# Optimization experiments

Hardware: AMD Instinct MI355X
Metric: run time of the kernel (lower is better)

Reference implementation:

```python
import jax, jax.numpy as jnp
import numpy as np

B, T, C, V, L, H, HS = 64, 256, 256, 65, 6, 8, 32


def _ln(x, g, b, eps=1e-5):
    mu = jnp.mean(x, axis=-1, keepdims=True)
    var = jnp.mean(jnp.square(x - mu), axis=-1, keepdims=True)
    return (x - mu) * jax.lax.rsqrt(var + eps) * g + b


def setup_inputs() -> dict:
    key = jax.random.key(0)
    ks = jax.random.split(key, 28)
    n = lambda k, s: jax.random.normal(k, s, dtype=jnp.float32) * 0.02
    return {
        "idx": jax.random.randint(ks[0], (B, T), 0, V),
        "targets": jax.random.randint(ks[1], (B, T), 0, V),
        "tok_emb": n(ks[2], (V, C)),
        "pos_emb": n(ks[3], (T, C)),
        "wq": n(ks[4], (L, H, C, HS)), "bq": n(ks[5], (L, H, HS)),
        "wk": n(ks[6], (L, H, C, HS)), "bk": n(ks[7], (L, H, HS)),
        "wv": n(ks[8], (L, H, C, HS)), "bv": n(ks[9], (L, H, HS)),
        "wo": n(ks[10], (L, C, C)), "bo": n(ks[11], (L, C)),
        "ln1_g": jnp.ones((L, C), jnp.float32), "ln1_b": jnp.zeros((L, C), jnp.float32),
        "w1": n(ks[12], (L, C, 4 * C)), "b1": n(ks[13], (L, 4 * C)),
        "w2": n(ks[14], (L, 4 * C, C)), "b2": n(ks[15], (L, C)),
        "ln2_g": jnp.ones((L, C), jnp.float32), "ln2_b": jnp.zeros((L, C), jnp.float32),
        "lnf_g": jnp.ones((C,), jnp.float32), "lnf_b": jnp.zeros((C,), jnp.float32),
        "lm_w": n(ks[16], (C, V)), "lm_b": n(ks[17], (V,)),
    }


def reference(idx, targets, tok_emb, pos_emb, wq, bq, wk, bk, wv, bv, wo, bo,
              ln1_g, ln1_b, w1, b1, w2, b2, ln2_g, ln2_b, lnf_g, lnf_b, lm_w, lm_b):
    Bc, Tc = idx.shape
    x = tok_emb[idx] + pos_emb[:Tc]  # [B,T,C]
    causal = jnp.tril(jnp.ones((Tc, Tc), dtype=bool))
    scale = C ** (-0.5)  # NOTE: original scales by n_embd**-0.5, not head_size
    for l in range(L):
        xn = _ln(x, ln1_g[l], ln1_b[l])
        q = jnp.einsum('btc,hcd->bhtd', xn, wq[l]) + bq[l][None, :, None, :]
        k = jnp.einsum('btc,hcd->bhtd', xn, wk[l]) + bk[l][None, :, None, :]
        v = jnp.einsum('btc,hcd->bhtd', xn, wv[l]) + bv[l][None, :, None, :]
        s = jnp.einsum('bhtd,bhsd->bhts', q, k) * scale
        s = jnp.where(causal, s, -jnp.inf)
        a = jax.nn.softmax(s, axis=-1)  # dropout is identity in eval
        o = jnp.einsum('bhts,bhsd->bhtd', a, v)
        o = o.transpose(0, 2, 1, 3).reshape(Bc, Tc, C)  # concat heads
        x = x + o @ wo[l] + bo[l]
        xn2 = _ln(x, ln2_g[l], ln2_b[l])
        h = jax.nn.relu(xn2 @ w1[l] + b1[l])
        x = x + h @ w2[l] + b2[l]
    x = _ln(x, lnf_g, lnf_b)
    logits = (x @ lm_w + lm_b).reshape(Bc * Tc, V)
    logp = jax.nn.log_softmax(logits, axis=-1)
    tgt = targets.reshape(-1)
    loss = -jnp.mean(logp[jnp.arange(Bc * Tc), tgt])
    return logits, loss
```

## Files before the change

### kernel.cpp

```cpp
#include <hip/hip_runtime.h>
#include <hip/hip_bf16.h>
#include <math.h>

#define BB 64
#define TT 256
#define CC 256
#define VV 65
#define LL 6
#define HH 8
#define BT (BB*TT)

typedef unsigned short u16;
typedef __attribute__((ext_vector_type(8))) _Float16 h8v;
typedef __attribute__((ext_vector_type(4))) float f4v;
typedef __attribute__((ext_vector_type(4))) unsigned short u16x4;

typedef const unsigned int __attribute__((address_space(1))) gu32;
typedef unsigned int       __attribute__((address_space(3))) lu32;

__device__ inline u16 f2h(float f) { _Float16 h = (_Float16)f; return *(u16*)&h; }

__device__ inline void gld_lds16(const void* g, void* l) {
    __builtin_amdgcn_global_load_lds((gu32*)g, (lu32*)l, 16, 0, 0);
}


__device__ inline void pack_dev(const float* __restrict__ src, u16* __restrict__ dst,
                                int K, int N, int NT, int KT, int id) {
    int perLayer = NT * KT * 8192;
    int l = id / perLayer; int rem = id - l * perLayer;
    int tile = rem >> 13, within = rem & 8191;
    int nT = tile / KT, kT = tile - nT * KT;
    int colIn = within >> 6, u = within & 63;
    int s = (u >> 3) ^ (colIn & 7);
    int k = kT * 64 + s * 8 + (u & 7);
    int n = nT * 128 + colIn;
    float v = (n < N) ? src[((size_t)l * K + k) * N + n] : 0.f;
    dst[((size_t)l * NT * KT + tile) * 8192 + within] = f2h(v);
}

#define E_QKV (LL*24*8192)
#define E_WO  (LL*8*8192)
#define E_W1  (LL*32*8192)
#define E_W2  (LL*32*8192)
#define E_LM  (4*8192)
#define E_QB  (LL*768)
#define E_TOT (E_QKV+E_WO+E_W1+E_W2+E_LM+E_QB)

__global__ __launch_bounds__(256)
void pack_all(const float* __restrict__ wq, const float* __restrict__ wk,
              const float* __restrict__ wv, const float* __restrict__ wo,
              const float* __restrict__ w1, const float* __restrict__ w2,
              const float* __restrict__ lmw,
              const float* __restrict__ bq, const float* __restrict__ bk,
              const float* __restrict__ bv,
              u16* __restrict__ qkvT, u16* __restrict__ woT, u16* __restrict__ w1T,
              u16* __restrict__ w2T, u16* __restrict__ lmT, float* __restrict__ Bp) {
    int id = blockIdx.x * 256 + threadIdx.x;
    if (id < E_QKV) {
        const int perLayer = 24 * 8192;
        int l = id / perLayer; int rem = id - l * perLayer;
        int tile = rem >> 13, within = rem & 8191;
        int nT = tile >> 2, kT = tile & 3;
        int colIn = within >> 6, u = within & 63;
        int s = (u >> 3) ^ (colIn & 7);
        int k = kT * 64 + s * 8 + (u & 7);
        int n = nT * 128 + colIn;
        int which = n >> 8, hd = n & 255, h = hd >> 5, d = hd & 31;
        const float* src = (which == 0) ? wq : (which == 1) ? wk : wv;
        float v = src[(((size_t)l * HH + h) * CC + k) * 32 + d];
        qkvT[((size_t)l * 24 + tile) * 8192 + within] = f2h(v);
        return;
    }
    id -= E_QKV;
    if (id < E_WO) { pack_dev(wo, woT, 256, 256, 2, 4, id); return; }
    id -= E_WO;
    if (id < E_W1) { pack_dev(w1, w1T, 256, 1024, 8, 4, id); return; }
    id -= E_W1;
    if (id < E_W2) { pack_dev(w2, w2T, 1024, 256, 2, 16, id); return; }
    id -= E_W2;
    if (id < E_LM) { pack_dev(lmw, lmT, 256, VV, 1, 4, id); return; }
    id -= E_LM;
    if (id < E_QB) {
        int l = id / 768, j = id % 768;
        int which = j >> 8, hd = j & 255, h = hd >> 5, d = hd & 31;
        const float* src = (which == 0) ? bq : (which == 1) ? bk : bv;
        Bp[id] = src[((size_t)l * HH + h) * 32 + d];
    }
}

__global__ __launch_bounds__(256)
void embed_kernel(const int* __restrict__ idx, const float* __restrict__ te,
                  const float* __restrict__ pe, float* __restrict__ x) {
    int i = blockIdx.x * blockDim.x + threadIdx.x;
    if (i >= BT * 64) return;
    int bt = i >> 6, c4 = i & 63;
    int tok = idx[bt];
    int t = bt & (TT - 1);
    float4 a = ((const float4*)te)[(size_t)tok * 64 + c4];
    float4 p = ((const float4*)pe)[(size_t)t * 64 + c4];
    float4 o; o.x = a.x + p.x; o.y = a.y + p.y; o.z = a.z + p.z; o.w = a.w + p.w;
    ((float4*)x)[i] = o;
}

__global__ __launch_bounds__(256)
void ln_kernel(const float* __restrict__ x, const float* __restrict__ g,
               const float* __restrict__ b, u16* __restrict__ outT) {
    int lane = threadIdx.x & 63;
    int wave = threadIdx.x >> 6;
    int row = blockIdx.x * 4 + wave;
    float4 v = ((const float4*)(x + (size_t)row * CC))[lane];
    float s = v.x + v.y + v.z + v.w;
    #pragma unroll
    for (int m = 1; m < 64; m <<= 1) s += __shfl_xor(s, m, 64);
    float mu = s * (1.f / CC);
    float dx = v.x - mu, dy = v.y - mu, dz = v.z - mu, dw = v.w - mu;
    float vs = dx * dx + dy * dy + dz * dz + dw * dw;
    #pragma unroll
    for (int m = 1; m < 64; m <<= 1) vs += __shfl_xor(vs, m, 64);
    float rs = rsqrtf(vs * (1.f / CC) + 1e-5f);
    float4 gv = ((const float4*)g)[lane];
    float4 bv = ((const float4*)b)[lane];
    float o[4];
    o[0] = dx * rs * gv.x + bv.x;
    o[1] = dy * rs * gv.y + bv.y;
    o[2] = dz * rs * gv.z + bv.z;
    o[3] = dw * rs * gv.w + bv.w;
    int rIn = row & 127, mT = row >> 7;
    int kT = lane >> 4;
    int kIn = (lane * 4) & 63;
    int slot = kIn >> 3, j = kIn & 7;
    size_t base = ((size_t)mT * 4 + kT) * 8192;
    int ub = rIn * 64 + ((slot ^ (rIn & 7)) << 3) + j;
    u16x4 hv;
    #pragma unroll
    for (int q = 0; q < 4; ++q) hv[q] = f2h(o[q]);
    *(u16x4*)(outT + base + ub) = hv;
}

template<int EPI>
__global__ __launch_bounds__(512, 4)
void gemm_mfma(const u16* __restrict__ At, const u16* __restrict__ Bt,
               const float* __restrict__ bias, float* __restrict__ Co,
               u16* __restrict__ CoT, int KTfull, int KTc, int NT, int N, int KTout) {
    __shared__ __align__(16) char lds[65536];
    int tid = threadIdx.x;
    int l = tid & 63, w = tid >> 6;
    int nwg = gridDim.x;
    int id = blockIdx.x;
    int cpx = nwg >> 3;
    id = (id & 7) * cpx + (id >> 3);
    int mT = id / NT, nT = id - mT * NT;
    int ktBase = blockIdx.y * KTc;

    const char* Abase = (const char*)(At + ((size_t)mT * KTfull + ktBase) * 8192);
    const char* Bbase = (const char*)(Bt + ((size_t)nT * KTfull + ktBase) * 8192);
    int wm = w >> 1, wn = w & 1;

    f4v acc[2][4];
    #pragma unroll
    for (int i = 0; i < 2; ++i)
        #pragma unroll
        for (int j = 0; j < 4; ++j) acc[i][j] = (f4v)0.f;

    int lrow = l & 15, lg = l >> 4;

    #define STAGE(buf, kt) {                                           \
        char* la = lds + (buf) * 32768 + w * 2048;                     \
        char* lb = lds + (buf) * 32768 + 16384 + w * 2048;             \
        const char* ga = Abase + (kt) * 16384 + w * 2048 + l * 16;     \
        const char* gb = Bbase + (kt) * 16384 + w * 2048 + l * 16;     \
        _Pragma("unroll")                                              \
        for (int j = 0; j < 2; ++j) {                                  \
            gld_lds16(ga + j * 1024, la + j * 1024);                   \
            gld_lds16(gb + j * 1024, lb + j * 1024);                   \
        } }

    STAGE(0, 0);
    __syncthreads();
    int cur = 0;
    for (int kt = 0; kt < KTc; ++kt) {
        if (kt + 1 < KTc) STAGE(cur ^ 1, kt + 1);
        const char* lb0 = lds + cur * 32768;
        #pragma unroll
        for (int kh = 0; kh < 2; ++kh) {
            h8v ah[2], bh[4];
            #pragma unroll
            for (int mi = 0; mi < 2; ++mi) {
                int rc = wm * 32 + mi * 16 + lrow;
                ah[mi] = *(const h8v*)(lb0 + rc * 128 + 16 * ((kh * 4 + lg) ^ (rc & 7)));
            }
            #pragma unroll
            for (int ni = 0; ni < 4; ++ni) {
                int rc = wn * 64 + ni * 16 + lrow;
                bh[ni] = *(const h8v*)(lb0 + 16384 + rc * 128 + 16 * ((kh * 4 + lg) ^ (rc & 7)));
            }
            #pragma unroll
            for (int mi = 0; mi < 2; ++mi)
                #pragma unroll
                for (int ni = 0; ni < 4; ++ni)
                    acc[mi][ni] = __builtin_amdgcn_mfma_f32_16x16x32_f16(ah[mi], bh[ni], acc[mi][ni], 0, 0, 0);
        }
        __syncthreads();
        cur ^= 1;
    }
    #undef STAGE

    int colbase = nT * 128 + wn * 64;
    if (EPI == 0) {
        #pragma unroll
        for (int mi = 0; mi < 2; ++mi) {
            int r0 = mT * 128 + wm * 32 + mi * 16 + lg * 4;
            #pragma unroll
            for (int ni = 0; ni < 4; ++ni) {
                int cg = colbase + ni * 16 + lrow;
                float bv = bias[cg];
                #pragma unroll
                for (int q = 0; q < 4; ++q)
                    CoT[(size_t)(r0 + q) * N + cg] = f2h(acc[mi][ni][q] + bv);
            }
        }
    } else if (EPI == 2) {
        #pragma unroll
        for (int mi = 0; mi < 2; ++mi) {
            int r0 = mT * 128 + wm * 32 + mi * 16 + lg * 4;
            #pragma unroll
            for (int ni = 0; ni < 4; ++ni) {
                int cg = colbase + ni * 16 + lrow;
                float bv = bias[cg];
                int kTo = cg >> 6, kIn = cg & 63;
                size_t tbase = ((size_t)mT * KTout + kTo) * 8192;
                #pragma unroll
                for (int q = 0; q < 4; ++q) {
                    int rIn = (r0 + q) & 127;
                    float f = fmaxf(acc[mi][ni][q] + bv, 0.f);
                    int ub = rIn * 64 + (((kIn >> 3) ^ (rIn & 7)) << 3) + (kIn & 7);
                    CoT[tbase + ub] = f2h(f);
                }
            }
        }
    } else if (EPI == 3) {
        #pragma unroll
        for (int mi = 0; mi < 2; ++mi) {
            int r0 = mT * 128 + wm * 32 + mi * 16 + lg * 4;
            #pragma unroll
            for (int ni = 0; ni < 4; ++ni) {
                int cg = colbase + ni * 16 + lrow;
                if (cg < VV) {
                    float bv = bias[cg];
                    #pragma unroll
                    for (int q = 0; q < 4; ++q)
                        Co[(size_t)(r0 + q) * VV + cg] = acc[mi][ni][q] + bv;
                }
            }
        }
    } else {
        #pragma unroll
        for (int mi = 0; mi < 2; ++mi) {
            int r0 = mT * 128 + wm * 32 + mi * 16 + lg * 4;
            #pragma unroll
            for (int ni = 0; ni < 4; ++ni) {
                int cg = colbase + ni * 16 + lrow;
                float bv = (ktBase == 0) ? bias[cg] : 0.f;
                #pragma unroll
                for (int q = 0; q < 4; ++q)
                    atomicAdd(Co + (size_t)(r0 + q) * N + cg, acc[mi][ni][q] + bv);
            }
        }
    }
}

__global__ __launch_bounds__(256)
void attn_mfma(const u16* __restrict__ qkv, u16* __restrict__ outT) {
    __shared__ __align__(16) char lds[42496];
    int bh = blockIdx.x;
    bh = (bh & 7) * 64 + (bh >> 3);
    int b = bh >> 3, h = bh & 7;
    const u16* base = qkv + (size_t)b * TT * 768;
    int tid = threadIdx.x;
    int w = tid >> 6, l = tid & 63;
    int li = l & 15, g = l >> 4;

    {
        int r0 = tid >> 3, c = tid & 7;
        #pragma unroll
        for (int it = 0; it < 8; ++it) {
            int t = it * 32 + r0;
            u16x4 kv = *(const u16x4*)(base + (size_t)t * 768 + 256 + h * 32 + c * 4);
            u16x4 vv = *(const u16x4*)(base + (size_t)t * 768 + 512 + h * 32 + c * 4);
            *(u16x4*)(lds + t * 80 + c * 8) = kv;
            *(u16*)(lds + 20480 + (c * 4 + 0) * 528 + t * 2) = vv[0];
            *(u16*)(lds + 20480 + (c * 4 + 1) * 528 + t * 2) = vv[1];
            *(u16*)(lds + 20480 + (c * 4 + 2) * 528 + t * 2) = vv[2];
            *(u16*)(lds + 20480 + (c * 4 + 3) * 528 + t * 2) = vv[3];
        }
    }
    __syncthreads();

    char* Pb = lds + 37376 + w * 1280;
    int mts[4] = {w, 7 - w, 8 + w, 15 - w};
    #pragma unroll
    for (int im = 0; im < 4; ++im) {
        int mt = mts[im];
        int mq = mt * 16;
        h8v aq = *(const h8v*)(base + (size_t)(mq + li) * 768 + h * 32 + g * 8);

        f4v o0 = (f4v)0.f, o1 = (f4v)0.f;
        float mrun0 = -1e30f, mrun1 = -1e30f, mrun2 = -1e30f, mrun3 = -1e30f;
        float lrun0 = 0.f, lrun1 = 0.f, lrun2 = 0.f, lrun3 = 0.f;
        int nu = (mt >> 1) + 1;
        for (int kt = 0; kt < nu; ++kt) {
            int kb = kt * 32;
            h8v kf0 = *(const h8v*)(lds + (kb + li) * 80 + g * 16);
            h8v kf1 = *(const h8v*)(lds + (kb + 16 + li) * 80 + g * 16);
            f4v s0 = __builtin_amdgcn_mfma_f32_16x16x32_f16(aq, kf0, (f4v)0.f, 0, 0, 0);
            f4v s1 = __builtin_amdgcn_mfma_f32_16x16x32_f16(aq, kf1, (f4v)0.f, 0, 0, 0);
            bool maskunit = (kt == nu - 1);
            float p0[4], p1[4];
            float* mr[4] = {&mrun0, &mrun1, &mrun2, &mrun3};
            float* lr[4] = {&lrun0, &lrun1, &lrun2, &lrun3};
            #pragma unroll
            for (int qq = 0; qq < 4; ++qq) {
                float v0 = s0[qq] * 0.0625f;
                float v1 = s1[qq] * 0.0625f;
                if (maskunit) {
                    int qg = mq + g * 4 + qq;
                    if (kb + li > qg)      v0 = -1e30f;
                    if (kb + 16 + li > qg) v1 = -1e30f;
                }
                float tm = fmaxf(v0, v1);
                #pragma unroll
                for (int msk = 1; msk < 16; msk <<= 1)
                    tm = fmaxf(tm, __shfl_xor(tm, msk, 64));
                float mold = *mr[qq];
                float mnew = fmaxf(mold, tm);
                float corr = __expf(mold - mnew);
                float e0 = __expf(v0 - mnew);
                float e1 = __expf(v1 - mnew);
                float ts = e0 + e1;
                #pragma unroll
                for (int msk = 1; msk < 16; msk <<= 1)
                    ts += __shfl_xor(ts, msk, 64);
                *lr[qq] = *lr[qq] * corr + ts;
                *mr[qq] = mnew;
                o0[qq] *= corr; o1[qq] *= corr;
                p0[qq] = e0; p1[qq] = e1;
            }
            #pragma unroll
            for (int qq = 0; qq < 4; ++qq) {
                *(u16*)(Pb + (g * 4 + qq) * 80 + li * 2)        = f2h(p0[qq]);
                *(u16*)(Pb + (g * 4 + qq) * 80 + (16 + li) * 2) = f2h(p1[qq]);
            }
            h8v pf  = *(const h8v*)(Pb + li * 80 + g * 16);
            h8v vf0 = *(const h8v*)(lds + 20480 + li * 528        + kb * 2 + g * 16);
            h8v vf1 = *(const h8v*)(lds + 20480 + (16 + li) * 528 + kb * 2 + g * 16);
            o0 = __builtin_amdgcn_mfma_f32_16x16x32_f16(pf, vf0, o0, 0, 0, 0);
            o1 = __builtin_amdgcn_mfma_f32_16x16x32_f16(pf, vf1, o1, 0, 0, 0);
        }
        float invs[4] = {1.f / lrun0, 1.f / lrun1, 1.f / lrun2, 1.f / lrun3};
        #pragma unroll
        for (int qq = 0; qq < 4; ++qq) {
            int tok = mq + g * 4 + qq;
            int rIn = tok & 127;
            size_t tb = ((size_t)(b * 2 + (tok >> 7)) * 4 + (h >> 1)) * 8192;
            float f0 = o0[qq] * invs[qq];
            float f1 = o1[qq] * invs[qq];
            int kIn0 = (h & 1) * 32 + li;
            int kIn1 = kIn0 + 16;
            int ub0 = rIn * 64 + (((kIn0 >> 3) ^ (rIn & 7)) << 3) + (kIn0 & 7);
            int ub1 = rIn * 64 + (((kIn1 >> 3) ^ (rIn & 7)) << 3) + (kIn1 & 7);
            outT[tb + ub0] = f2h(f0);
            outT[tb + ub1] = f2h(f1);
        }
    }
}

__global__ __launch_bounds__(256)
void loss_kernel(const float* __restrict__ lg, const int* __restrict__ tgt,
                 float* __restrict__ loss) {
    int row = blockIdx.x * 256 + threadIdx.x;
    const float* r = lg + (size_t)row * VV;
    float mx = -INFINITY;
    for (int v = 0; v < VV; ++v) mx = fmaxf(mx, r[v]);
    float se = 0.f;
    for (int v = 0; v < VV; ++v) se += __expf(r[v] - mx);
    float nl = mx + __logf(se) - r[tgt[row]];
    #pragma unroll
    for (int m = 1; m < 64; m <<= 1) nl += __shfl_xor(nl, m, 64);
    __shared__ float wsum[4];
    int lane = threadIdx.x & 63, wv = threadIdx.x >> 6;
    if (lane == 0) wsum[wv] = nl;
    __syncthreads();
    if (threadIdx.x == 0)
        atomicAdd(loss, (wsum[0] + wsum[1] + wsum[2] + wsum[3]) * (1.f / BT));
}

extern "C" void kernel_launch(void* const* d_in, const int* in_sizes, int n_in,
                              void* d_out, int out_size, void* d_ws, size_t ws_size,
                              hipStream_t stream) {
    const int*   idx  = (const int*)d_in[0];
    const int*   tgt  = (const int*)d_in[1];
    const float* te   = (const float*)d_in[2];
    const float* pe   = (const float*)d_in[3];
    const float* wq   = (const float*)d_in[4];
    const float* bq   = (const float*)d_in[5];
    const float* wk   = (const float*)d_in[6];
    const float* bk   = (const float*)d_in[7];
    const float* wv   = (const float*)d_in[8];
    const float* bv   = (const float*)d_in[9];
    const float* wo   = (const float*)d_in[10];
    const float* bo   = (const float*)d_in[11];
    const float* ln1g = (const float*)d_in[12];
    const float* ln1b = (const float*)d_in[13];
    const float* w1   = (const float*)d_in[14];
    const float* b1   = (const float*)d_in[15];
    const float* w2   = (const float*)d_in[16];
    const float* b2   = (const float*)d_in[17];
    const float* ln2g = (const float*)d_in[18];
    const float* ln2b = (const float*)d_in[19];
    const float* lnfg = (const float*)d_in[20];
    const float* lnfb = (const float*)d_in[21];
    const float* lmw  = (const float*)d_in[22];
    const float* lmb  = (const float*)d_in[23];
    float* out = (float*)d_out;

    char* base = (char*)d_ws;
    float* x       = (float*)(base);
    u16*   qkvh    = (u16*)  (base + (16ll << 20));
    u16*   hiddenT = (u16*)  (base + (40ll << 20));
    u16*   xnT     = (u16*)  (base + (72ll << 20));
    u16*   qkvT    = (u16*)  (base + (80ll << 20));
    u16*   woT     = (u16*)  (base + (83ll << 20));
    u16*   w1T     = (u16*)  (base + (84ll << 20));
    u16*   w2T     = (u16*)  (base + (87ll << 20));
    u16*   lmT     = (u16*)  (base + (90ll << 20));
    float* Bp      = (float*)(base + (91ll << 20));

    pack_all<<<dim3(E_TOT / 256), 256, 0, stream>>>(wq, wk, wv, wo, w1, w2, lmw,
                                                    bq, bk, bv,
                                                    qkvT, woT, w1T, w2T, lmT, Bp);
    embed_kernel<<<dim3((BT * 64) / 256), 256, 0, stream>>>(idx, te, pe, x);

    for (int l = 0; l < LL; ++l) {
        ln_kernel<<<dim3(BT / 4), 256, 0, stream>>>(x, ln1g + l * CC, ln1b + l * CC, xnT);
        gemm_mfma<0><<<dim3(128 * 6, 1), 512, 0, stream>>>(
            xnT, qkvT + (size_t)l * 196608, Bp + l * 768, nullptr, qkvh, 4, 4, 6, 768, 0);
        attn_mfma<<<dim3(BB * HH), 256, 0, stream>>>(qkvh, xnT);
        gemm_mfma<4><<<dim3(128 * 2, 2), 512, 0, stream>>>(
            xnT, woT + (size_t)l * 65536, bo + l * CC, x, nullptr, 4, 2, 2, 256, 0);
        ln_kernel<<<dim3(BT / 4), 256, 0, stream>>>(x, ln2g + l * CC, ln2b + l * CC, xnT);
        gemm_mfma<2><<<dim3(128 * 8, 1), 512, 0, stream>>>(
            xnT, w1T + (size_t)l * 262144, b1 + l * 1024, nullptr, hiddenT, 4, 4, 8, 1024, 16);
        gemm_mfma<4><<<dim3(128 * 2, 2), 512, 0, stream>>>(
            hiddenT, w2T + (size_t)l * 262144, b2 + l * CC, x, nullptr, 16, 8, 2, 256, 0);
    }
    ln_kernel<<<dim3(BT / 4), 256, 0, stream>>>(x, lnfg, lnfb, xnT);
    gemm_mfma<3><<<dim3(128 * 1, 1), 512, 0, stream>>>(
        xnT, lmT, lmb, out, nullptr, 4, 4, 1, VV, 0);

    hipMemsetAsync(out + (size_t)BT * VV, 0, sizeof(float), stream);
    loss_kernel<<<dim3(BT / 256), 256, 0, stream>>>(out, tgt, out + (size_t)BT * VV);
}
```

Before: 980.4 us.

## Replace split-K atomic accumulation with partial buffers reduced inside fused residual+LayerNorm

The split-K GEMMs for the attention output and MLP down projections now write plain stores of their partial sums into two separate buffers instead of issuing atomicAdd into the residual stream. A new sum_ln kernel adds both partials plus the bias to the residual, writes the residual back, and emits the fp16 LayerNorm output in one pass. This removes atomic contention and folds the residual update into the following LayerNorm. In exchange it costs extra global memory traffic, since it writes and rereads two fp32 partial buffers per GEMM.

```diff
diff --git a/kernel.cpp b/kernel.cpp
--- a/kernel.cpp
+++ b/kernel.cpp
@@ -103,13 +103,9 @@
     ((float4*)x)[i] = o;
 }
 
-__global__ __launch_bounds__(256)
-void ln_kernel(const float* __restrict__ x, const float* __restrict__ g,
-               const float* __restrict__ b, u16* __restrict__ outT) {
-    int lane = threadIdx.x & 63;
-    int wave = threadIdx.x >> 6;
-    int row = blockIdx.x * 4 + wave;
-    float4 v = ((const float4*)(x + (size_t)row * CC))[lane];
+__device__ inline void ln_emit(float4 v, const float* __restrict__ g,
+                               const float* __restrict__ b, u16* __restrict__ outT,
+                               int row, int lane) {
     float s = v.x + v.y + v.z + v.w;
     #pragma unroll
     for (int m = 1; m < 64; m <<= 1) s += __shfl_xor(s, m, 64);
@@ -121,11 +117,6 @@
     float rs = rsqrtf(vs * (1.f / CC) + 1e-5f);
     float4 gv = ((const float4*)g)[lane];
     float4 bv = ((const float4*)b)[lane];
-    float o[4];
-    o[0] = dx * rs * gv.x + bv.x;
-    o[1] = dy * rs * gv.y + bv.y;
-    o[2] = dz * rs * gv.z + bv.z;
-    o[3] = dw * rs * gv.w + bv.w;
     int rIn = row & 127, mT = row >> 7;
     int kT = lane >> 4;
     int kIn = (lane * 4) & 63;
@@ -133,9 +124,40 @@
     size_t base = ((size_t)mT * 4 + kT) * 8192;
     int ub = rIn * 64 + ((slot ^ (rIn & 7)) << 3) + j;
     u16x4 hv;
-    #pragma unroll
-    for (int q = 0; q < 4; ++q) hv[q] = f2h(o[q]);
+    hv[0] = f2h(dx * rs * gv.x + bv.x);
+    hv[1] = f2h(dy * rs * gv.y + bv.y);
+    hv[2] = f2h(dz * rs * gv.z + bv.z);
+    hv[3] = f2h(dw * rs * gv.w + bv.w);
     *(u16x4*)(outT + base + ub) = hv;
+}
+
+__global__ __launch_bounds__(256)
+void ln_kernel(const float* __restrict__ x, const float* __restrict__ g,
+               const float* __restrict__ b, u16* __restrict__ outT) {
+    int lane = threadIdx.x & 63;
+    int row = blockIdx.x * 4 + (threadIdx.x >> 6);
+    float4 v = ((const float4*)(x + (size_t)row * CC))[lane];
+    ln_emit(v, g, b, outT, row, lane);
+}
+
+__global__ __launch_bounds__(256)
+void sum_ln(float* __restrict__ x, const float* __restrict__ p0,
+            const float* __restrict__ p1, const float* __restrict__ gbias,
+            const float* __restrict__ g, const float* __restrict__ b,
+            u16* __restrict__ outT) {
+    int lane = threadIdx.x & 63;
+    int row = blockIdx.x * 4 + (threadIdx.x >> 6);
+    size_t off = (size_t)row * CC;
+    float4 v  = ((const float4*)(x + off))[lane];
+    float4 a0 = ((const float4*)(p0 + off))[lane];
+    float4 a1 = ((const float4*)(p1 + off))[lane];
+    float4 bb = ((const float4*)gbias)[lane];
+    v.x += a0.x + a1.x + bb.x;
+    v.y += a0.y + a1.y + bb.y;
+    v.z += a0.z + a1.z + bb.z;
+    v.w += a0.w + a1.w + bb.w;
+    ((float4*)(x + off))[lane] = v;
+    ln_emit(v, g, b, outT, row, lane);
 }
 
 template<int EPI>
@@ -255,16 +277,16 @@
             }
         }
     } else {
+        float* P = Co + (size_t)blockIdx.y * ((size_t)BT * N);
         #pragma unroll
         for (int mi = 0; mi < 2; ++mi) {
             int r0 = mT * 128 + wm * 32 + mi * 16 + lg * 4;
             #pragma unroll
             for (int ni = 0; ni < 4; ++ni) {
                 int cg = colbase + ni * 16 + lrow;
-                float bv = (ktBase == 0) ? bias[cg] : 0.f;
                 #pragma unroll
                 for (int q = 0; q < 4; ++q)
-                    atomicAdd(Co + (size_t)(r0 + q) * N + cg, acc[mi][ni][q] + bv);
+                    P[(size_t)(r0 + q) * N + cg] = acc[mi][ni][q];
             }
         }
     }
@@ -435,6 +457,8 @@
     u16*   w2T     = (u16*)  (base + (87ll << 20));
     u16*   lmT     = (u16*)  (base + (90ll << 20));
     float* Bp      = (float*)(base + (91ll << 20));
+    float* Pbuf    = (float*)(base + (96ll << 20));
+    float* Qbuf    = (float*)(base + (128ll << 20));
 
     pack_all<<<dim3(E_TOT / 256), 256, 0, stream>>>(wq, wk, wv, wo, w1, w2, lmw,
                                                     bq, bk, bv,
@@ -442,19 +466,27 @@
     embed_kernel<<<dim3((BT * 64) / 256), 256, 0, stream>>>(idx, te, pe, x);
 
     for (int l = 0; l < LL; ++l) {
-        ln_kernel<<<dim3(BT / 4), 256, 0, stream>>>(x, ln1g + l * CC, ln1b + l * CC, xnT);
+        if (l == 0)
+            ln_kernel<<<dim3(BT / 4), 256, 0, stream>>>(x, ln1g, ln1b, xnT);
+        else
+            sum_ln<<<dim3(BT / 4), 256, 0, stream>>>(x, Qbuf, Qbuf + (size_t)BT * CC,
+                                                     b2 + (l - 1) * CC,
+                                                     ln1g + l * CC, ln1b + l * CC, xnT);
         gemm_mfma<0><<<dim3(128 * 6, 1), 512, 0, stream>>>(
             xnT, qkvT + (size_t)l * 196608, Bp + l * 768, nullptr, qkvh, 4, 4, 6, 768, 0);
         attn_mfma<<<dim3(BB * HH), 256, 0, stream>>>(qkvh, xnT);
         gemm_mfma<4><<<dim3(128 * 2, 2), 512, 0, stream>>>(
-            xnT, woT + (size_t)l * 65536, bo + l * CC, x, nullptr, 4, 2, 2, 256, 0);
-        ln_kernel<<<dim3(BT / 4), 256, 0, stream>>>(x, ln2g + l * CC, ln2b + l * CC, xnT);
+            xnT, woT + (size_t)l * 65536, nullptr, Pbuf, nullptr, 4, 2, 2, 256, 0);
+        sum_ln<<<dim3(BT / 4), 256, 0, stream>>>(x, Pbuf, Pbuf + (size_t)BT * CC,
+                                                 bo + l * CC,
+                                                 ln2g + l * CC, ln2b + l * CC, xnT);
         gemm_mfma<2><<<dim3(128 * 8, 1), 512, 0, stream>>>(
             xnT, w1T + (size_t)l * 262144, b1 + l * 1024, nullptr, hiddenT, 4, 4, 8, 1024, 16);
         gemm_mfma<4><<<dim3(128 * 2, 2), 512, 0, stream>>>(
-            hiddenT, w2T + (size_t)l * 262144, b2 + l * CC, x, nullptr, 16, 8, 2, 256, 0);
-    }
-    ln_kernel<<<dim3(BT / 4), 256, 0, stream>>>(x, lnfg, lnfb, xnT);
+            hiddenT, w2T + (size_t)l * 262144, nullptr, Qbuf, nullptr, 16, 8, 2, 256, 0);
+    }
+    sum_ln<<<dim3(BT / 4), 256, 0, stream>>>(x, Qbuf, Qbuf + (size_t)BT * CC,
+                                             b2 + (LL - 1) * CC, lnfg, lnfb, xnT);
     gemm_mfma<3><<<dim3(128 * 1, 1), 512, 0, stream>>>(
         xnT, lmT, lmb, out, nullptr, 4, 4, 1, VV, 0);
 
```

Measured after the change: 816.7 us. -16.7%, faster.
